# Kernel optimization log

Hardware: AMD Instinct MI355X
Metric: run time of the kernel (lower is better)

Reference implementation:

```python
import jax, jax.numpy as jnp
import numpy as np

B, D, U1, U2 = 16384, 512, 512, 512
BN_EPS = 1e-3  # keras BatchNormalization default epsilon


def sparsemax(z):
    # z: [..., D]; standard sparsemax along last axis (Martins & Astudillo)
    d = z.shape[-1]
    z_sorted = -jnp.sort(-z, axis=-1)                      # descending
    z_cum = jnp.cumsum(z_sorted, axis=-1)
    k = jnp.arange(1, d + 1, dtype=z.dtype)
    support = (1.0 + k * z_sorted) > z_cum                 # [..., D] bool
    k_z = jnp.sum(support, axis=-1, keepdims=True)         # support size
    tau = (jnp.take_along_axis(z_cum, k_z.astype(jnp.int32) - 1, axis=-1) - 1.0) / k_z.astype(z.dtype)
    return jnp.maximum(z - tau, 0.0)


def setup_inputs() -> dict:
    key = jax.random.key(0)
    ks = jax.random.split(key, 8)
    x = jax.random.normal(ks[0], (B, D), dtype=jnp.float32)
    W1 = jax.random.normal(ks[1], (D, U1), dtype=jnp.float32) * 0.05
    b1 = jnp.zeros((U1,), jnp.float32)
    centers = jax.random.normal(ks[2], (U2, D), dtype=jnp.float32)      # paraboloid centers
    coefs = jax.random.normal(ks[3], (U2, D), dtype=jnp.float32) * 0.1  # paraboloid axis coefficients
    bn_gamma = jnp.ones((D,), jnp.float32)
    bn_beta = jnp.zeros((D,), jnp.float32)
    bn_mean = jnp.zeros((D,), jnp.float32)
    bn_var = jnp.ones((D,), jnp.float32)
    W_out = jax.random.normal(ks[4], (U1 + U2, D), dtype=jnp.float32) * 0.05
    b_out = jnp.zeros((D,), jnp.float32)
    w_add = jnp.array([0.5, 0.5], jnp.float32)  # WeightedAdd learnable scalars
    return {"x": x, "W1": W1, "b1": b1, "centers": centers, "coefs": coefs,
            "bn_gamma": bn_gamma, "bn_beta": bn_beta, "bn_mean": bn_mean, "bn_var": bn_var,
            "W_out": W_out, "b_out": b_out, "w_add": w_add}


def reference(x, W1, b1, centers, coefs, bn_gamma, bn_beta, bn_mean, bn_var, W_out, b_out, w_add):
    # Dense branch
    h1 = jax.nn.relu(x @ W1 + b1)                               # [B, U1]
    # BoundedParaboloids branch: BatchNorm (inference stats) then bounded paraboloids
    xb = (x - bn_mean) * jax.lax.rsqrt(bn_var + BN_EPS) * bn_gamma + bn_beta
    # q_j = sum_d (coefs[j,d] * (xb_d - centers[j,d]))^2, computed via GEMMs
    A = coefs * coefs                                            # [U2, D]
    q = (xb * xb) @ A.T - 2.0 * (xb @ (A * centers).T) + jnp.sum(A * centers * centers, axis=-1)
    h2 = jax.nn.relu(1.0 - q)                                    # [B, U2] bounded paraboloids
    # Output embedding: Dense(relu) on concat
    emb = jax.nn.relu(jnp.concatenate([h1, h2], axis=-1) @ W_out + b_out)  # [B, D]
    # WeightedAdd of (dropout-identity) inputs and embedding; dropout_rate=0 / inference
    pre = w_add[0] * x + w_add[1] * emb
    mask = sparsemax(pre)                                        # [B, D]
    return mask
```

## Files before the change

kernel.cpp:

```cpp
#include <hip/hip_runtime.h>
#include <math.h>

typedef float f4 __attribute__((ext_vector_type(4)));
typedef float f32x4 __attribute__((ext_vector_type(4)));
typedef __bf16 bf16x8 __attribute__((ext_vector_type(8)));
typedef unsigned short u16;
typedef u16 us8 __attribute__((ext_vector_type(8)));

__device__ __forceinline__ u16 f2bf(float f) {
  unsigned u = __builtin_bit_cast(unsigned, f);
  unsigned r = u + 0x7fffu + ((u >> 16) & 1u);
  return (u16)(r >> 16);
}
__device__ __forceinline__ float bf2f(u16 h) {
  unsigned u = ((unsigned)h) << 16;
  return __builtin_bit_cast(float, u);
}

__global__ __launch_bounds__(256) void prep_bn_kernel(
    const float* __restrict__ gamma, const float* __restrict__ beta,
    const float* __restrict__ mean, const float* __restrict__ var,
    float* __restrict__ scale, float* __restrict__ shift) {
  int d = blockIdx.x * blockDim.x + threadIdx.x;
  if (d < 512) {
    float s = rsqrtf(var[d] + 1e-3f) * gamma[d];
    scale[d] = s;
    shift[d] = beta[d] - mean[d] * s;
  }
}

__global__ __launch_bounds__(64) void prep_params_kernel(
    const float* __restrict__ coefs, const float* __restrict__ centers,
    u16* __restrict__ pth, float* __restrict__ cvec) {
  int j = blockIdx.x;
  int l = threadIdx.x;
  int d0 = l * 8;
  f4 c0 = *(const f4*)(coefs + (size_t)j * 512 + d0);
  f4 c1 = *(const f4*)(coefs + (size_t)j * 512 + d0 + 4);
  f4 e0 = *(const f4*)(centers + (size_t)j * 512 + d0);
  f4 e1 = *(const f4*)(centers + (size_t)j * 512 + d0 + 4);
  us8 pa, pb;
  float acc = 0.f;
#pragma unroll
  for (int e = 0; e < 8; ++e) {
    float cf = (e < 4) ? c0[e] : c1[e - 4];
    float ce = (e < 4) ? e0[e] : e1[e - 4];
    float a = cf * cf;
    pa[e] = f2bf(a);
    pb[e] = f2bf(-2.f * a * ce);
    acc = fmaf(a * ce, ce, acc);
  }
  *(us8*)(pth + (size_t)j * 1024 + d0) = pa;
  *(us8*)(pth + (size_t)j * 1024 + 512 + d0) = pb;
#pragma unroll
  for (int off = 32; off; off >>= 1) acc += __shfl_xor(acc, off);
  if (l == 0) cvec[j] = acc;
}

__global__ __launch_bounds__(256) void transpose_split_kernel(
    const float* __restrict__ in, u16* __restrict__ th, u16* __restrict__ tl,
    int K, int N) {
  __shared__ float t[32][33];
  int lx = threadIdx.x;
  int ly = threadIdx.y;
  int n0 = blockIdx.x * 32, k0 = blockIdx.y * 32;
#pragma unroll
  for (int i = 0; i < 4; ++i)
    t[ly + 8 * i][lx] = in[(size_t)(k0 + ly + 8 * i) * N + n0 + lx];
  __syncthreads();
#pragma unroll
  for (int i = 0; i < 4; ++i) {
    float v = t[lx][ly + 8 * i];
    u16 h = f2bf(v);
    u16 lo = f2bf(v - bf2f(h));
    th[(size_t)(n0 + ly + 8 * i) * K + k0 + lx] = h;
    tl[(size_t)(n0 + ly + 8 * i) * K + k0 + lx] = lo;
  }
}

__global__ __launch_bounds__(256) void conv_x_kernel(
    const float* __restrict__ x, const float* __restrict__ scale,
    const float* __restrict__ shift, u16* __restrict__ xh,
    u16* __restrict__ xb) {
  int gid = blockIdx.x * 256 + threadIdx.x;
  int m = gid >> 6;
  int d0 = (gid & 63) * 8;
  f4 v0 = *(const f4*)(x + (size_t)m * 512 + d0);
  f4 v1 = *(const f4*)(x + (size_t)m * 512 + d0 + 4);
  f4 s0 = *(const f4*)(scale + d0);
  f4 s1 = *(const f4*)(scale + d0 + 4);
  f4 h0 = *(const f4*)(shift + d0);
  f4 h1 = *(const f4*)(shift + d0 + 4);
  us8 oh, ob;
#pragma unroll
  for (int e = 0; e < 8; ++e) {
    float xv = (e < 4) ? v0[e] : v1[e - 4];
    float sc = (e < 4) ? s0[e] : s1[e - 4];
    float sh = (e < 4) ? h0[e] : h1[e - 4];
    oh[e] = f2bf(xv);
    ob[e] = f2bf(fmaf(xv, sc, sh));
  }
  *(us8*)(xh + (size_t)m * 512 + d0) = oh;
  *(us8*)(xb + (size_t)m * 512 + d0) = ob;
}

__global__ __launch_bounds__(256, 4) void gemm_fused12(
    const u16* __restrict__ Xh, const u16* __restrict__ Xb,
    const u16* __restrict__ W1th, const u16* __restrict__ Pth,
    const float* __restrict__ b1, const float* __restrict__ cvec,
    u16* __restrict__ Hout) {
  extern __shared__ char smem[];
  char* sA = smem;
  char* sBh = smem + 16384;
  const int tid = threadIdx.x;
  const int l = tid & 63;
  const int w = tid >> 6;
  const int wm = w & 1, wn = w >> 1;
  const int lr = l & 15, lk = l >> 4;
  const int sx = lr & 7;
  const int bid = blockIdx.x;
  const int L = (bid & 7) * 128 + (bid >> 3);
  const int p = L >> 3;
  const int g = (L >> 2) & 1;
  const int n = L & 3;
  const int m0 = p * 128, n0 = n * 128;
  const int Kg = g ? 1024 : 512;
  const u16* Bmat = g ? Pth : W1th;
  const u16* Amat = g ? Xb : Xh;
  const int srow = l >> 3;
  const int sslot = (l & 7) ^ srow;

  f32x4 acc[4][4];
#pragma unroll
  for (int i = 0; i < 4; ++i)
#pragma unroll
    for (int j = 0; j < 4; ++j) acc[i][j] = (f32x4){0.f, 0.f, 0.f, 0.f};

  for (int k0 = 0; k0 < Kg; k0 += 64) {
#pragma unroll
    for (int pp = 0; pp < 4; ++pp) {
      int c = pp * 4 + w;
      int row = c * 8 + srow;
      int loff = c * 1024;
      size_t gob = (size_t)(n0 + row) * Kg + k0 + sslot * 8;
      __builtin_amdgcn_global_load_lds(
          (const __attribute__((address_space(1))) void*)(Bmat + gob),
          (__attribute__((address_space(3))) void*)(sBh + loff), 16, 0, 0);
      if (g) {
        int kb = (k0 < 512) ? k0 : (k0 - 512);
        us8 v = *(const us8*)(Amat + (size_t)(m0 + row) * 512 + kb + sslot * 8);
        us8 o;
        if (k0 < 512) {
#pragma unroll
          for (int e = 0; e < 8; ++e) {
            float f = bf2f(v[e]);
            o[e] = f2bf(f * f);
          }
        } else {
          o = v;
        }
        *(us8*)(sA + loff + l * 16) = o;
      } else {
        size_t goa = (size_t)(m0 + row) * 512 + k0 + sslot * 8;
        __builtin_amdgcn_global_load_lds(
            (const __attribute__((address_space(1))) void*)(Amat + goa),
            (__attribute__((address_space(3))) void*)(sA + loff), 16, 0, 0);
      }
    }
    __syncthreads();
#pragma unroll
    for (int ks = 0; ks < 2; ++ks) {
      bf16x8 av[4], bv[4];
#pragma unroll
      for (int i = 0; i < 4; ++i)
        av[i] = *(const bf16x8*)(sA + (wm * 64 + i * 16 + lr) * 128 +
                                 (((ks * 4 + lk) ^ sx) * 16));
#pragma unroll
      for (int j = 0; j < 4; ++j)
        bv[j] = *(const bf16x8*)(sBh + (wn * 64 + j * 16 + lr) * 128 +
                                 (((ks * 4 + lk) ^ sx) * 16));
#pragma unroll
      for (int i = 0; i < 4; ++i)
#pragma unroll
        for (int j = 0; j < 4; ++j)
          acc[i][j] = __builtin_amdgcn_mfma_f32_16x16x32_bf16(av[i], bv[j],
                                                              acc[i][j], 0, 0, 0);
    }
    __syncthreads();
  }

  const int mwb = m0 + wm * 64;
  const int nwb = n0 + wn * 64;
  const float* bias = g ? cvec : b1;
#pragma unroll
  for (int j = 0; j < 4; ++j) {
    int nn = nwb + j * 16 + lr;
    float bv = bias[nn];
#pragma unroll
    for (int i = 0; i < 4; ++i) {
#pragma unroll
      for (int r = 0; r < 4; ++r) {
        int m = mwb + i * 16 + lk * 4 + r;
        float v = acc[i][j][r] + bv;
        v = g ? fmaxf(1.f - v, 0.f) : fmaxf(v, 0.f);
        Hout[(size_t)m * 1024 + g * 512 + nn] = f2bf(v);
      }
    }
  }
}

__global__ __launch_bounds__(256, 2) void gemm3(
    const u16* __restrict__ Ah, const u16* __restrict__ Bh,
    const u16* __restrict__ Bl, const float* __restrict__ bias,
    const float* __restrict__ xorig, const float* __restrict__ wadd,
    float* __restrict__ outp) {
  extern __shared__ char smem[];
  char* sA = smem;
  char* sBh = smem + 16384;
  char* sBl = smem + 32768;
  const int tid = threadIdx.x;
  const int l = tid & 63;
  const int w = tid >> 6;
  const int wm = w & 1, wn = w >> 1;
  const int lr = l & 15, lk = l >> 4;
  const int sx = lr & 7;
  const int bid = blockIdx.x;
  const int lin = (bid & 7) * 64 + (bid >> 3);
  const int m0 = (lin >> 2) * 128, n0 = (lin & 3) * 128;
  const int srow = l >> 3;
  const int sslot = (l & 7) ^ srow;

  f32x4 acc[4][4];
#pragma unroll
  for (int i = 0; i < 4; ++i)
#pragma unroll
    for (int j = 0; j < 4; ++j) acc[i][j] = (f32x4){0.f, 0.f, 0.f, 0.f};

  for (int k0 = 0; k0 < 1024; k0 += 64) {
    const bool lo = (k0 < 512);
#pragma unroll
    for (int pp = 0; pp < 4; ++pp) {
      int c = pp * 4 + w;
      int row = c * 8 + srow;
      int loff = c * 1024;
      size_t gob = (size_t)(n0 + row) * 1024 + k0 + sslot * 8;
      size_t goa = (size_t)(m0 + row) * 1024 + k0 + sslot * 8;
      __builtin_amdgcn_global_load_lds(
          (const __attribute__((address_space(1))) void*)(Bh + gob),
          (__attribute__((address_space(3))) void*)(sBh + loff), 16, 0, 0);
      __builtin_amdgcn_global_load_lds(
          (const __attribute__((address_space(1))) void*)(Ah + goa),
          (__attribute__((address_space(3))) void*)(sA + loff), 16, 0, 0);
      if (lo) {
        __builtin_amdgcn_global_load_lds(
            (const __attribute__((address_space(1))) void*)(Bl + gob),
            (__attribute__((address_space(3))) void*)(sBl + loff), 16, 0, 0);
      }
    }
    __syncthreads();
#pragma unroll
    for (int ks = 0; ks < 2; ++ks) {
      bf16x8 av[4], bv[4];
#pragma unroll
      for (int i = 0; i < 4; ++i)
        av[i] = *(const bf16x8*)(sA + (wm * 64 + i * 16 + lr) * 128 +
                                 (((ks * 4 + lk) ^ sx) * 16));
#pragma unroll
      for (int j = 0; j < 4; ++j)
        bv[j] = *(const bf16x8*)(sBh + (wn * 64 + j * 16 + lr) * 128 +
                                 (((ks * 4 + lk) ^ sx) * 16));
#pragma unroll
      for (int i = 0; i < 4; ++i)
#pragma unroll
        for (int j = 0; j < 4; ++j)
          acc[i][j] = __builtin_amdgcn_mfma_f32_16x16x32_bf16(av[i], bv[j],
                                                              acc[i][j], 0, 0, 0);
      if (lo) {
#pragma unroll
        for (int j = 0; j < 4; ++j)
          bv[j] = *(const bf16x8*)(sBl + (wn * 64 + j * 16 + lr) * 128 +
                                   (((ks * 4 + lk) ^ sx) * 16));
#pragma unroll
        for (int i = 0; i < 4; ++i)
#pragma unroll
          for (int j = 0; j < 4; ++j)
            acc[i][j] = __builtin_amdgcn_mfma_f32_16x16x32_bf16(
                av[i], bv[j], acc[i][j], 0, 0, 0);
      }
    }
    __syncthreads();
  }

  const int mwb = m0 + wm * 64;
  const int nwb = n0 + wn * 64;
  float w0 = wadd[0], w1 = wadd[1];
#pragma unroll
  for (int j = 0; j < 4; ++j) {
    int n = nwb + j * 16 + lr;
    float bv = bias[n];
#pragma unroll
    for (int i = 0; i < 4; ++i) {
#pragma unroll
      for (int r = 0; r < 4; ++r) {
        int m = mwb + i * 16 + lk * 4 + r;
        float v = fmaxf(acc[i][j][r] + bv, 0.f);
        outp[(size_t)m * 512 + n] = fmaf(w1, v, w0 * xorig[(size_t)m * 512 + n]);
      }
    }
  }
}

__global__ __launch_bounds__(256) void sparsemax_kernel(float* __restrict__ out) {
  int row = blockIdx.x * 4 + (threadIdx.x >> 6);
  int lane = threadIdx.x & 63;
  float* rp = out + (size_t)row * 512;
  f4 z0 = *(const f4*)(rp + lane * 8);
  f4 z1 = *(const f4*)(rp + lane * 8 + 4);
  float z[8];
#pragma unroll
  for (int e = 0; e < 4; ++e) {
    z[e] = z0[e];
    z[4 + e] = z1[e];
  }
  float m = z[0];
#pragma unroll
  for (int i = 1; i < 8; ++i) m = fmaxf(m, z[i]);
#pragma unroll
  for (int off = 32; off; off >>= 1) m = fmaxf(m, __shfl_xor(m, off));
  float tau = m - 1.0f;
  for (int it = 0; it < 32; ++it) {
    float s = 0.f, k = 0.f;
#pragma unroll
    for (int i = 0; i < 8; ++i) {
      if (z[i] > tau) {
        s += z[i] - tau;
        k += 1.f;
      }
    }
#pragma unroll
    for (int off = 32; off; off >>= 1) {
      s += __shfl_xor(s, off);
      k += __shfl_xor(k, off);
    }
    if (k < 0.5f) break;
    float tn = tau + (s - 1.f) / k;
    if (tn == tau) break;
    tau = tn;
  }
  float s = 0.f, k = 0.f;
#pragma unroll
  for (int i = 0; i < 8; ++i)
    if (z[i] > tau) {
      s += z[i];
      k += 1.f;
    }
#pragma unroll
  for (int off = 32; off; off >>= 1) {
    s += __shfl_xor(s, off);
    k += __shfl_xor(k, off);
  }
  float tauf = (k >= 0.5f) ? (s - 1.f) / k : (m - 1.f);
  f4 o0, o1;
#pragma unroll
  for (int e = 0; e < 4; ++e) {
    o0[e] = fmaxf(z[e] - tauf, 0.f);
    o1[e] = fmaxf(z[4 + e] - tauf, 0.f);
  }
  *(f4*)(rp + lane * 8) = o0;
  *(f4*)(rp + lane * 8 + 4) = o1;
}

extern "C" void kernel_launch(void* const* d_in, const int* in_sizes, int n_in,
                              void* d_out, int out_size, void* d_ws,
                              size_t ws_size, hipStream_t stream) {
  const float* x = (const float*)d_in[0];
  const float* W1 = (const float*)d_in[1];
  const float* b1 = (const float*)d_in[2];
  const float* centers = (const float*)d_in[3];
  const float* coefs = (const float*)d_in[4];
  const float* gamma = (const float*)d_in[5];
  const float* beta = (const float*)d_in[6];
  const float* mean = (const float*)d_in[7];
  const float* var = (const float*)d_in[8];
  const float* W_out = (const float*)d_in[9];
  const float* b_out = (const float*)d_in[10];
  const float* wadd = (const float*)d_in[11];
  float* out = (float*)d_out;

  char* ws = (char*)d_ws;
  u16* Hh = (u16*)(ws);
  u16* Xh = (u16*)(ws + 33554432);
  u16* Xb = (u16*)(ws + 50331648);
  char* pool = ws + 67108864;
  u16* W1th = (u16*)(pool);
  u16* W1tl = (u16*)(pool + 524288);
  u16* Pth = (u16*)(pool + 1048576);
  u16* Wth = (u16*)(pool);
  u16* Wtl = (u16*)(pool + 1048576);
  float* cvec = (float*)(ws + 69206016);
  float* scale = (float*)(ws + 69208064);
  float* shift = (float*)(ws + 69210112);

  prep_bn_kernel<<<2, 256, 0, stream>>>(gamma, beta, mean, var, scale, shift);
  prep_params_kernel<<<512, 64, 0, stream>>>(coefs, centers, Pth, cvec);
  transpose_split_kernel<<<dim3(16, 16), dim3(32, 8), 0, stream>>>(W1, W1th,
                                                                   W1tl, 512,
                                                                   512);
  conv_x_kernel<<<4096, 256, 0, stream>>>(x, scale, shift, Xh, Xb);

  gemm_fused12<<<1024, 256, 32768, stream>>>(Xh, Xb, W1th, Pth, b1, cvec, Hh);

  transpose_split_kernel<<<dim3(16, 32), dim3(32, 8), 0, stream>>>(W_out, Wth,
                                                                   Wtl, 1024,
                                                                   512);
  gemm3<<<512, 256, 49152, stream>>>(Hh, Wth, Wtl, b_out, x, wadd, out);
  sparsemax_kernel<<<4096, 256, 0, stream>>>(out);
}
```

Baseline: 122.3 us.

## Drop W_out low-part split GEMM, double-buffer gemm3 loads, reorder fused12 blocks

The output GEMM no longer uses the bf16 hi/lo split of W_out for its first half of K, which removes a third of its MFMAs and global loads. The freed shared memory is used to double-buffer the A/B tiles, so the next K-slice is fetched while the current one is computed. The transpose kernel skips writing low parts when given a null pointer. gemm_fused12 also flips which block slots get the long-K paraboloid work. Dropping the split lowers the precision of the h1 contribution to emb, which could shift sparsemax supports near ties.

```diff
diff --git a/kernel.cpp b/kernel.cpp
--- a/kernel.cpp
+++ b/kernel.cpp
@@ -72,9 +72,11 @@
   for (int i = 0; i < 4; ++i) {
     float v = t[lx][ly + 8 * i];
     u16 h = f2bf(v);
-    u16 lo = f2bf(v - bf2f(h));
     th[(size_t)(n0 + ly + 8 * i) * K + k0 + lx] = h;
-    tl[(size_t)(n0 + ly + 8 * i) * K + k0 + lx] = lo;
+    if (tl) {
+      u16 lo = f2bf(v - bf2f(h));
+      tl[(size_t)(n0 + ly + 8 * i) * K + k0 + lx] = lo;
+    }
   }
 }
 
@@ -121,7 +123,7 @@
   const int bid = blockIdx.x;
   const int L = (bid & 7) * 128 + (bid >> 3);
   const int p = L >> 3;
-  const int g = (L >> 2) & 1;
+  const int g = ((L >> 2) & 1) ^ 1;
   const int n = L & 3;
   const int m0 = p * 128, n0 = n * 128;
   const int Kg = g ? 1024 : 512;
@@ -211,13 +213,9 @@
 
 __global__ __launch_bounds__(256, 2) void gemm3(
     const u16* __restrict__ Ah, const u16* __restrict__ Bh,
-    const u16* __restrict__ Bl, const float* __restrict__ bias,
-    const float* __restrict__ xorig, const float* __restrict__ wadd,
-    float* __restrict__ outp) {
+    const float* __restrict__ bias, const float* __restrict__ xorig,
+    const float* __restrict__ wadd, float* __restrict__ outp) {
   extern __shared__ char smem[];
-  char* sA = smem;
-  char* sBh = smem + 16384;
-  char* sBl = smem + 32768;
   const int tid = threadIdx.x;
   const int l = tid & 63;
   const int w = tid >> 6;
@@ -236,28 +234,31 @@
 #pragma unroll
     for (int j = 0; j < 4; ++j) acc[i][j] = (f32x4){0.f, 0.f, 0.f, 0.f};
 
-  for (int k0 = 0; k0 < 1024; k0 += 64) {
-    const bool lo = (k0 < 512);
-#pragma unroll
-    for (int pp = 0; pp < 4; ++pp) {
-      int c = pp * 4 + w;
-      int row = c * 8 + srow;
-      int loff = c * 1024;
-      size_t gob = (size_t)(n0 + row) * 1024 + k0 + sslot * 8;
-      size_t goa = (size_t)(m0 + row) * 1024 + k0 + sslot * 8;
-      __builtin_amdgcn_global_load_lds(
-          (const __attribute__((address_space(1))) void*)(Bh + gob),
-          (__attribute__((address_space(3))) void*)(sBh + loff), 16, 0, 0);
-      __builtin_amdgcn_global_load_lds(
-          (const __attribute__((address_space(1))) void*)(Ah + goa),
-          (__attribute__((address_space(3))) void*)(sA + loff), 16, 0, 0);
-      if (lo) {
-        __builtin_amdgcn_global_load_lds(
-            (const __attribute__((address_space(1))) void*)(Bl + gob),
-            (__attribute__((address_space(3))) void*)(sBl + loff), 16, 0, 0);
-      }
-    }
-    __syncthreads();
+#define G3_STAGE(buf, k0)                                                     \
+  {                                                                           \
+    char* dA = smem + (buf)*16384;                                            \
+    char* dB = smem + 32768 + (buf)*16384;                                    \
+    _Pragma("unroll") for (int pp = 0; pp < 4; ++pp) {                        \
+      int c = pp * 4 + w;                                                     \
+      int row = c * 8 + srow;                                                 \
+      int loff = c * 1024;                                                    \
+      size_t gob = (size_t)(n0 + row) * 1024 + (k0) + sslot * 8;              \
+      size_t goa = (size_t)(m0 + row) * 1024 + (k0) + sslot * 8;              \
+      __builtin_amdgcn_global_load_lds(                                       \
+          (const __attribute__((address_space(1))) void*)(Bh + gob),          \
+          (__attribute__((address_space(3))) void*)(dB + loff), 16, 0, 0);    \
+      __builtin_amdgcn_global_load_lds(                                       \
+          (const __attribute__((address_space(1))) void*)(Ah + goa),          \
+          (__attribute__((address_space(3))) void*)(dA + loff), 16, 0, 0);    \
+    }                                                                         \
+  }
+
+  G3_STAGE(0, 0);
+  __syncthreads();
+  for (int t = 0; t < 16; ++t) {
+    if (t + 1 < 16) G3_STAGE((t + 1) & 1, (t + 1) * 64);
+    const char* sA = smem + (t & 1) * 16384;
+    const char* sB = smem + 32768 + (t & 1) * 16384;
 #pragma unroll
     for (int ks = 0; ks < 2; ++ks) {
       bf16x8 av[4], bv[4];
@@ -267,7 +268,7 @@
                                  (((ks * 4 + lk) ^ sx) * 16));
 #pragma unroll
       for (int j = 0; j < 4; ++j)
-        bv[j] = *(const bf16x8*)(sBh + (wn * 64 + j * 16 + lr) * 128 +
+        bv[j] = *(const bf16x8*)(sB + (wn * 64 + j * 16 + lr) * 128 +
                                  (((ks * 4 + lk) ^ sx) * 16));
 #pragma unroll
       for (int i = 0; i < 4; ++i)
@@ -275,21 +276,10 @@
         for (int j = 0; j < 4; ++j)
           acc[i][j] = __builtin_amdgcn_mfma_f32_16x16x32_bf16(av[i], bv[j],
                                                               acc[i][j], 0, 0, 0);
-      if (lo) {
-#pragma unroll
-        for (int j = 0; j < 4; ++j)
-          bv[j] = *(const bf16x8*)(sBl + (wn * 64 + j * 16 + lr) * 128 +
-                                   (((ks * 4 + lk) ^ sx) * 16));
-#pragma unroll
-        for (int i = 0; i < 4; ++i)
-#pragma unroll
-          for (int j = 0; j < 4; ++j)
-            acc[i][j] = __builtin_amdgcn_mfma_f32_16x16x32_bf16(
-                av[i], bv[j], acc[i][j], 0, 0, 0);
-      }
     }
     __syncthreads();
   }
+#undef G3_STAGE
 
   const int mwb = m0 + wm * 64;
   const int nwb = n0 + wn * 64;
@@ -393,26 +383,22 @@
   u16* Xb = (u16*)(ws + 50331648);
   char* pool = ws + 67108864;
   u16* W1th = (u16*)(pool);
-  u16* W1tl = (u16*)(pool + 524288);
   u16* Pth = (u16*)(pool + 1048576);
   u16* Wth = (u16*)(pool);
-  u16* Wtl = (u16*)(pool + 1048576);
   float* cvec = (float*)(ws + 69206016);
   float* scale = (float*)(ws + 69208064);
   float* shift = (float*)(ws + 69210112);
 
   prep_bn_kernel<<<2, 256, 0, stream>>>(gamma, beta, mean, var, scale, shift);
   prep_params_kernel<<<512, 64, 0, stream>>>(coefs, centers, Pth, cvec);
-  transpose_split_kernel<<<dim3(16, 16), dim3(32, 8), 0, stream>>>(W1, W1th,
-                                                                   W1tl, 512,
-                                                                   512);
+  transpose_split_kernel<<<dim3(16, 16), dim3(32, 8), 0, stream>>>(
+      W1, W1th, nullptr, 512, 512);
   conv_x_kernel<<<4096, 256, 0, stream>>>(x, scale, shift, Xh, Xb);
 
   gemm_fused12<<<1024, 256, 32768, stream>>>(Xh, Xb, W1th, Pth, b1, cvec, Hh);
 
-  transpose_split_kernel<<<dim3(16, 32), dim3(32, 8), 0, stream>>>(W_out, Wth,
-                                                                   Wtl, 1024,
-                                                                   512);
-  gemm3<<<512, 256, 49152, stream>>>(Hh, Wth, Wtl, b_out, x, wadd, out);
+  transpose_split_kernel<<<dim3(16, 32), dim3(32, 8), 0, stream>>>(
+      W_out, Wth, nullptr, 1024, 512);
+  gemm3<<<512, 256, 65536, stream>>>(Hh, Wth, b_out, x, wadd, out);
   sparsemax_kernel<<<4096, 256, 0, stream>>>(out);
 }
```

New measurement: 114.0 us. 1.07x faster.
